# Kernel tuning notes

Hardware: AMD Instinct MI355X
Metric: run time of the kernel (lower is better)

## Reference

```python
import jax, jax.numpy as jnp
import numpy as np

H_DIM = 2048
N_HEADS = 16
HEAD_DIM = H_DIM // N_HEADS
B, S = 2, 2048


def setup_inputs() -> dict:
    key = jax.random.key(0)
    ks = jax.random.split(key, 10)
    sc = 1.0 / np.sqrt(H_DIM)
    return {
        "X": jax.random.normal(ks[0], (B, S, H_DIM), dtype=jnp.float32),
        "attention_mask": jnp.ones((B, S, S), dtype=jnp.int32),
        "Wq": jax.random.normal(ks[1], (H_DIM, H_DIM), dtype=jnp.float32) * sc,
        "bq": jnp.zeros((H_DIM,), dtype=jnp.float32),
        "Wk": jax.random.normal(ks[2], (H_DIM, H_DIM), dtype=jnp.float32) * sc,
        "bk": jnp.zeros((H_DIM,), dtype=jnp.float32),
        "Wv": jax.random.normal(ks[3], (H_DIM, H_DIM), dtype=jnp.float32) * sc,
        "bv": jnp.zeros((H_DIM,), dtype=jnp.float32),
        "Wo": jax.random.normal(ks[4], (H_DIM, H_DIM), dtype=jnp.float32) * sc,
        "bo": jnp.zeros((H_DIM,), dtype=jnp.float32),
    }


def reference(X, attention_mask, Wq, bq, Wk, bk, Wv, bv, Wo, bo):
    b, s, _ = X.shape
    # QKV projections -> [b, heads, s, head_dim]
    def proj(W, bias):
        y = jnp.einsum("bsd,de->bse", X, W) + bias
        return y.reshape(b, s, N_HEADS, HEAD_DIM).transpose(0, 2, 1, 3)
    Q, K, V = proj(Wq, bq), proj(Wk, bk), proj(Wv, bv)
    # scores [b, h, s, s]
    scores = jnp.einsum("bhqd,bhkd->bhqk", Q, K) / jnp.sqrt(jnp.float32(HEAD_DIM))
    mask = attention_mask[:, None, :, :]  # [b,1,s,s]
    scores = jnp.where(mask == 0, jnp.float32(-jnp.inf), scores)
    attn = jax.nn.softmax(scores, axis=-1)
    # dropout_rate = 0.0 -> no-op
    out = jnp.einsum("bhqk,bhkd->bhqd", attn, V)
    out = out.transpose(0, 2, 1, 3).reshape(b, s, H_DIM)
    return jnp.einsum("bsd,de->bse", out, Wo) + bo
```

## Files before the change

kernel.cpp:

```cpp
#include <hip/hip_runtime.h>
#include <hip/hip_bf16.h>

#define H_DIM 2048
#define N_HEADS 16
#define HEAD_DIM 128
#define BATCH 2
#define SEQ 2048

typedef __bf16 bf16_t;
typedef __bf16 bf16x8 __attribute__((ext_vector_type(8)));
typedef float f32x4 __attribute__((ext_vector_type(4)));

#define MFMA16(a, b, c) __builtin_amdgcn_mfma_f32_16x16x32_bf16((a), (b), (c), 0, 0, 0)

#define GLOAD16(gp, lp) __builtin_amdgcn_global_load_lds( \
    (const __attribute__((address_space(1))) void*)(gp),  \
    (__attribute__((address_space(3))) void*)(lp), 16, 0, 0)

#define WAIT_VM6()  asm volatile("s_waitcnt vmcnt(6)" ::: "memory")
#define WAIT_VM4()  asm volatile("s_waitcnt vmcnt(4)" ::: "memory")
#define WAIT_VM0()  asm volatile("s_waitcnt vmcnt(0)" ::: "memory")
#define RAW_BARRIER() asm volatile("s_barrier" ::: "memory")

__global__ __launch_bounds__(256) void detect_kernel(const unsigned int* __restrict__ X,
                                                     int* __restrict__ flags) {
    __shared__ int cnt[256];
    int t = threadIdx.x;
    int c = 0;
    for (int i = 0; i < 16; i++) {
        unsigned w  = X[t * 16 + i];
        unsigned lo = w & 0xFFFFu;
        unsigned e  = (lo >> 7) & 0xFFu;
        if (lo == 0u || (e >= 100u && e <= 141u)) c++;
    }
    cnt[t] = c;
    __syncthreads();
    for (int s = 128; s > 0; s >>= 1) {
        if (t < s) cnt[t] += cnt[t + s];
        __syncthreads();
    }
    if (t == 0) { flags[0] = (cnt[0] >= 2048) ? 1 : 0; flags[1] = 1; }
}

__global__ __launch_bounds__(256) void maskcheck_kernel(const int* __restrict__ mask,
                                                        int* __restrict__ flags) {
    size_t i = ((size_t)blockIdx.x * 256 + threadIdx.x) * 8;
    const int4* p = (const int4*)(mask + i);
    int4 a = p[0], b = p[1];
    int all = (a.x != 0) & (a.y != 0) & (a.z != 0) & (a.w != 0) &
              (b.x != 0) & (b.y != 0) & (b.z != 0) & (b.w != 0);
    if (!all) atomicAnd(&flags[1], 0);
}

__device__ inline bf16x8 load8(const void* __restrict__ p, size_t idx, int isbf16) {
    if (isbf16) {
        return *(const bf16x8*)((const bf16_t*)p + idx);
    } else {
        const float* f = (const float*)p + idx;
        float4 a = *(const float4*)f;
        float4 b = *(const float4*)(f + 4);
        bf16x8 r;
        r[0] = (bf16_t)a.x; r[1] = (bf16_t)a.y; r[2] = (bf16_t)a.z; r[3] = (bf16_t)a.w;
        r[4] = (bf16_t)b.x; r[5] = (bf16_t)b.y; r[6] = (bf16_t)b.z; r[7] = (bf16_t)b.w;
        return r;
    }
}

__device__ inline float readf(const void* __restrict__ p, int idx, int isbf16) {
    return isbf16 ? (float)((const bf16_t*)p)[idx] : ((const float*)p)[idx];
}

__global__ __launch_bounds__(256) void convert_kernel(const void* __restrict__ X,
                                                      bf16_t* __restrict__ Xb,
                                                      const int* __restrict__ flags) {
    const int isbf16 = flags[0];
    size_t i = ((size_t)blockIdx.x * 256 + threadIdx.x) * 8;
    bf16x8 v = load8(X, i, isbf16);
    *(bf16x8*)(Xb + i) = v;
}

__global__ __launch_bounds__(256) void transpose_kernel(
    const void* __restrict__ W0, const void* __restrict__ W1,
    const void* __restrict__ W2, const void* __restrict__ W3,
    bf16_t* __restrict__ Wts, const int* __restrict__ flags)
{
    const int isbf16 = flags[0];
    const int z = blockIdx.z;
    const void* W = (z == 0) ? W0 : (z == 1) ? W1 : (z == 2) ? W2 : W3;
    bf16_t* out = Wts + (size_t)z * H_DIM * H_DIM;

    __shared__ __attribute__((aligned(16))) bf16_t Ts[64][72];
    const int tid = threadIdx.x;
    const int n0 = blockIdx.x * 64;
    const int k0 = blockIdx.y * 64;

    #pragma unroll
    for (int j = 0; j < 2; j++) {
        int idx = j * 2048 + tid * 8;
        int r = idx >> 6, c = idx & 63;
        bf16x8 v = load8(W, (size_t)(k0 + r) * H_DIM + n0 + c, isbf16);
        *(bf16x8*)(&Ts[r][c]) = v;
    }
    __syncthreads();
    const int wr = tid & 63;
    const int wcg = (tid >> 6) * 8;
    #pragma unroll
    for (int j = 0; j < 2; j++) {
        int wc = wcg + j * 32;
        bf16x8 o;
        #pragma unroll
        for (int u = 0; u < 8; u++) o[u] = Ts[wc + u][wr];
        *(bf16x8*)(&out[(size_t)(n0 + wr) * H_DIM + k0 + wc]) = o;
    }
}

__global__ __launch_bounds__(256, 2) void gemm_qkv_kernel(
    const bf16_t* __restrict__ A, const bf16_t* __restrict__ Wts,
    const void* __restrict__ b0, const void* __restrict__ b1, const void* __restrict__ b2,
    bf16_t* __restrict__ qws, bf16_t* __restrict__ kws, bf16_t* __restrict__ vtws,
    const int* __restrict__ flags)
{
    const int isbf16 = flags[0];
    const int L    = blockIdx.x;
    const int xcd  = L & 7;
    const int j    = L >> 3;
    const int c    = xcd * 6 + (j % 6);
    const int mrow = j / 6;
    const int z    = c >> 4;
    const int m0   = mrow * 256;
    const int n0   = (c & 15) * 128;

    const bf16_t* Wt = Wts + (size_t)z * H_DIM * H_DIM;
    const void* bias = (z == 0) ? b0 : (z == 1) ? b1 : b2;
    bf16_t* dst = (z == 0) ? qws : (z == 1) ? kws : vtws;

    __shared__ __attribute__((aligned(16))) bf16_t As[3][4][256][8];
    __shared__ __attribute__((aligned(16))) bf16_t Bs[3][4][128][8];

    const int tid  = threadIdx.x;
    const int lane = tid & 63;
    const int wid  = tid >> 6;
    const int quad = lane >> 4;
    const int l16  = lane & 15;
    const int wm   = (wid >> 1) * 128;
    const int wn   = (wid & 1) * 64;

    f32x4 acc[8][4] = {};

    auto stage = [&](int k0, int sb) {
        #pragma unroll
        for (int jj = 0; jj < 4; jj++) {
            int slot = jj * 256 + tid;
            int k8 = slot >> 8, row = slot & 255;
            GLOAD16(A + (size_t)(m0 + row) * H_DIM + k0 + k8 * 8,
                    (bf16_t*)(&As[sb][0][0][0]) + slot * 8);
        }
        #pragma unroll
        for (int jj = 0; jj < 2; jj++) {
            int slot = jj * 256 + tid;
            int k8 = slot >> 7, row = slot & 127;
            GLOAD16(Wt + (size_t)(n0 + row) * H_DIM + k0 + k8 * 8,
                    (bf16_t*)(&Bs[sb][0][0][0]) + slot * 8);
        }
    };

    auto body = [&](int it, int bb, int sb, int mode) {
        if (mode == 2) { WAIT_VM0(); } else { WAIT_VM6(); }
        RAW_BARRIER();
        if (mode == 0) stage((it + 2) * 32, sb);
        bf16x8 bfr[4];
        #pragma unroll
        for (int i = 0; i < 4; i++)
            bfr[i] = *(const bf16x8*)(&Bs[bb][quad][wn + i * 16 + l16][0]);
        #pragma unroll
        for (int mi = 0; mi < 8; mi++) {
            bf16x8 af = *(const bf16x8*)(&As[bb][quad][wm + mi * 16 + l16][0]);
            #pragma unroll
            for (int ni = 0; ni < 4; ni++)
                acc[mi][ni] = MFMA16(af, bfr[ni], acc[mi][ni]);
        }
    };

    stage(0, 0);
    stage(32, 1);
    for (int base = 0; base < 60; base += 3) {
        body(base,     0, 2, 0);
        body(base + 1, 1, 0, 0);
        body(base + 2, 2, 1, 0);
    }
    body(60, 0, 2, 0);
    body(61, 1, 0, 0);
    body(62, 2, 1, 1);
    body(63, 0, 0, 2);

    #pragma unroll
    for (int ni = 0; ni < 4; ni++) {
        int col = n0 + wn + ni * 16 + l16;
        int h = col >> 7, d = col & (HEAD_DIM - 1);
        float bv = readf(bias, col, isbf16);
        #pragma unroll
        for (int mi = 0; mi < 8; mi++) {
            int row0 = m0 + wm + mi * 16 + quad * 4;
            int b = row0 >> 11;
            if (z < 2) {
                #pragma unroll
                for (int r = 0; r < 4; r++) {
                    int s = (row0 + r) & (SEQ - 1);
                    dst[((size_t)(b * N_HEADS + h) * SEQ + s) * HEAD_DIM + d] =
                        (bf16_t)(acc[mi][ni][r] + bv);
                }
            } else {
                int s0 = row0 & (SEQ - 1);
                bf16_t o[4];
                #pragma unroll
                for (int r = 0; r < 4; r++) o[r] = (bf16_t)(acc[mi][ni][r] + bv);
                *(unsigned long long*)(&dst[((size_t)(b * N_HEADS + h) * HEAD_DIM + d) * SEQ + s0]) =
                    *(unsigned long long*)o;
            }
        }
    }
}

__global__ __launch_bounds__(256) void gemm_out_kernel(
    const bf16_t* __restrict__ A, const bf16_t* __restrict__ Wt,
    const void* __restrict__ bias, void* __restrict__ C,
    const int* __restrict__ flags)
{
    const int isbf16 = flags[0];
    const int L    = blockIdx.x;
    const int xcd  = L & 7;
    const int j    = L >> 3;
    const int m0   = (j >> 1) * 128;
    const int n0   = (xcd * 2 + (j & 1)) * 128;

    __shared__ __attribute__((aligned(16))) bf16_t As[3][4][128][8];
    __shared__ __attribute__((aligned(16))) bf16_t Bs[3][4][128][8];

    const int tid  = threadIdx.x;
    const int lane = tid & 63;
    const int wid  = tid >> 6;
    const int quad = lane >> 4;
    const int l16  = lane & 15;
    const int wm   = (wid >> 1) * 64;
    const int wn   = (wid & 1) * 64;

    f32x4 acc[4][4] = {};

    auto stage = [&](int k0, int sb) {
        #pragma unroll
        for (int jj = 0; jj < 2; jj++) {
            int slot = jj * 256 + tid;
            int k8 = slot >> 7, row = slot & 127;
            GLOAD16(A  + (size_t)(m0 + row) * H_DIM + k0 + k8 * 8,
                    (bf16_t*)(&As[sb][0][0][0]) + slot * 8);
            GLOAD16(Wt + (size_t)(n0 + row) * H_DIM + k0 + k8 * 8,
                    (bf16_t*)(&Bs[sb][0][0][0]) + slot * 8);
        }
    };

    auto body = [&](int it, int bb, int sb, int mode) {
        if (mode == 2) { WAIT_VM0(); } else { WAIT_VM4(); }
        RAW_BARRIER();
        if (mode == 0) stage((it + 2) * 32, sb);
        bf16x8 af[4], bfr[4];
        #pragma unroll
        for (int i = 0; i < 4; i++) {
            af[i]  = *(const bf16x8*)(&As[bb][quad][wm + i * 16 + l16][0]);
            bfr[i] = *(const bf16x8*)(&Bs[bb][quad][wn + i * 16 + l16][0]);
        }
        #pragma unroll
        for (int mi = 0; mi < 4; mi++)
            #pragma unroll
            for (int ni = 0; ni < 4; ni++)
                acc[mi][ni] = MFMA16(af[mi], bfr[ni], acc[mi][ni]);
    };

    stage(0, 0);
    stage(32, 1);
    for (int base = 0; base < 60; base += 3) {
        body(base,     0, 2, 0);
        body(base + 1, 1, 0, 0);
        body(base + 2, 2, 1, 0);
    }
    body(60, 0, 2, 0);
    body(61, 1, 0, 0);
    body(62, 2, 1, 1);
    body(63, 0, 0, 2);

    #pragma unroll
    for (int ni = 0; ni < 4; ni++) {
        int col = n0 + wn + ni * 16 + l16;
        float bv = readf(bias, col, isbf16);
        #pragma unroll
        for (int mi = 0; mi < 4; mi++) {
            int row0 = m0 + wm + mi * 16 + quad * 4;
            #pragma unroll
            for (int r = 0; r < 4; r++) {
                float v = acc[mi][ni][r] + bv;
                if (isbf16) ((bf16_t*)C)[(size_t)(row0 + r) * H_DIM + col] = (bf16_t)v;
                else        ((float*)C)[(size_t)(row0 + r) * H_DIM + col]  = v;
            }
        }
    }
}

__global__ __launch_bounds__(256, 2) void attn_kernel(
    const bf16_t* __restrict__ Q, const bf16_t* __restrict__ K,
    const bf16_t* __restrict__ Vt, const int* __restrict__ mask,
    const int* __restrict__ flags, bf16_t* __restrict__ ctx)
{
    __shared__ __attribute__((aligned(16))) bf16_t Ks[2][16][64][8];
    __shared__ __attribute__((aligned(16))) bf16_t Vs[2][8][128][8];
    __shared__ __attribute__((aligned(16))) bf16_t Pl[4][16][72];

    const int tid  = threadIdx.x;
    const int lane = tid & 63;
    const int wid  = tid >> 6;
    const int quad = lane >> 4;
    const int l16  = lane & 15;

    const int bh = blockIdx.y;
    const int b  = bh >> 4, h = bh & 15;
    const int q0 = blockIdx.x * 128 + wid * 16;
    const int q1 = q0 + 64;
    const int maskAll = flags[1];

    const bf16_t* Qp = Q  + (size_t)bh * SEQ * HEAD_DIM;
    const bf16_t* Kp = K  + (size_t)bh * SEQ * HEAD_DIM;
    const bf16_t* Vp = Vt + (size_t)bh * HEAD_DIM * SEQ;
    const int*    mp = mask + (size_t)b * SEQ * SEQ;

    bf16x8 qf[2][4];
    #pragma unroll
    for (int t = 0; t < 4; t++) {
        qf[0][t] = *(const bf16x8*)(Qp + (size_t)(q0 + l16) * HEAD_DIM + t * 32 + quad * 8);
        qf[1][t] = *(const bf16x8*)(Qp + (size_t)(q1 + l16) * HEAD_DIM + t * 32 + quad * 8);
    }

    bf16x8 onesf;
    #pragma unroll
    for (int u = 0; u < 8; u++) onesf[u] = (bf16_t)1.0f;

    const float CS = 0.1275260013f;
    const float M0 = 16.0f;
    f32x4 l_acc[2] = {};
    f32x4 o_acc[2][8] = {};

    auto stage = [&](int kt, int bb) {
        const int key0 = kt * 64;
        #pragma unroll
        for (int jj = 0; jj < 4; jj++) {
            int slot = jj * 256 + tid;
            int krow = slot & 63, k8 = slot >> 6;
            GLOAD16(Kp + (size_t)(key0 + krow) * HEAD_DIM + k8 * 8,
                    (bf16_t*)(&Ks[bb][0][0][0]) + slot * 8);
        }
        #pragma unroll
        for (int jj = 0; jj < 4; jj++) {
            int slot = jj * 256 + tid;
            int d = slot & 127, kq = slot >> 7;
            GLOAD16(Vp + (size_t)d * SEQ + key0 + kq * 8,
                    (bf16_t*)(&Vs[bb][0][0][0]) + slot * 8);
        }
    };

    const int NKT = SEQ / 64;

    auto abody = [&](int kt, int bb) {
        const int key0 = kt * 64;
        __syncthreads();
        if (kt + 1 < NKT) stage(kt + 1, bb ^ 1);

        f32x4 s0[4] = {}, s1[4] = {};
        #pragma unroll
        for (int nt = 0; nt < 4; nt++) {
            #pragma unroll
            for (int t = 0; t < 4; t++) {
                bf16x8 kf = *(const bf16x8*)(&Ks[bb][t * 4 + quad][nt * 16 + l16][0]);
                s0[nt] = MFMA16(qf[0][t], kf, s0[nt]);
                s1[nt] = MFMA16(qf[1][t], kf, s1[nt]);
            }
        }

        #pragma unroll
        for (int u = 0; u < 2; u++) {
            float p2[4][4];
            #pragma unroll
            for (int nt = 0; nt < 4; nt++)
                #pragma unroll
                for (int r = 0; r < 4; r++)
                    p2[nt][r] = (u ? s1[nt][r] : s0[nt][r]) * CS - M0;

            if (!maskAll) {
                int qb = u ? q1 : q0;
                #pragma unroll
                for (int nt = 0; nt < 4; nt++) {
                    int key = key0 + nt * 16 + l16;
                    #pragma unroll
                    for (int r = 0; r < 4; r++) {
                        int q = qb + quad * 4 + r;
                        if (mp[(size_t)q * SEQ + key] == 0) p2[nt][r] = -1e30f;
                    }
                }
            }

            #pragma unroll
            for (int nt = 0; nt < 4; nt++)
                #pragma unroll
                for (int r = 0; r < 4; r++)
                    Pl[wid][quad * 4 + r][nt * 16 + l16] = (bf16_t)exp2f(p2[nt][r]);

            #pragma unroll
            for (int t = 0; t < 2; t++) {
                bf16x8 pf = *(const bf16x8*)(&Pl[wid][l16][t * 32 + quad * 8]);
                l_acc[u] = MFMA16(pf, onesf, l_acc[u]);
                #pragma unroll
                for (int dn = 0; dn < 8; dn++) {
                    bf16x8 vf = *(const bf16x8*)(&Vs[bb][t * 4 + quad][dn * 16 + l16][0]);
                    o_acc[u][dn] = MFMA16(pf, vf, o_acc[u][dn]);
                }
            }
        }
    };

    stage(0, 0);
    for (int base = 0; base < NKT; base += 2) {
        abody(base, 0);
        abody(base + 1, 1);
    }

    #pragma unroll
    for (int u = 0; u < 2; u++) {
        int qb = u ? q1 : q0;
        #pragma unroll
        for (int dn = 0; dn < 8; dn++) {
            #pragma unroll
            for (int r = 0; r < 4; r++) {
                int q = qb + quad * 4 + r;
                int d = dn * 16 + l16;
                float v = o_acc[u][dn][r] / l_acc[u][r];
                ctx[((size_t)(b * SEQ + q) * N_HEADS + h) * HEAD_DIM + d] = (bf16_t)v;
            }
        }
    }
}

extern "C" void kernel_launch(void* const* d_in, const int* in_sizes, int n_in,
                              void* d_out, int out_size, void* d_ws, size_t ws_size,
                              hipStream_t stream) {
    const void* X    = d_in[0];
    const int*  mask = (const int*)d_in[1];
    const void* Wq   = d_in[2];
    const void* bq   = d_in[3];
    const void* Wk   = d_in[4];
    const void* bk   = d_in[5];
    const void* Wv   = d_in[6];
    const void* bv   = d_in[7];
    const void* Wo   = d_in[8];
    const void* bo   = d_in[9];

    const size_t NE = (size_t)BATCH * SEQ * H_DIM;
    const size_t NW = (size_t)H_DIM * H_DIM;

    int*    flags = (int*)d_ws;
    bf16_t* Xb    = (bf16_t*)((char*)d_ws + 256);
    bf16_t* Wts   = Xb + NE;
    bf16_t* qws   = Wts + 4 * NW;
    bf16_t* kws   = qws + NE;
    bf16_t* vtws  = kws + NE;
    bf16_t* cws   = vtws + NE;

    detect_kernel<<<1, 256, 0, stream>>>((const unsigned int*)X, flags);
    maskcheck_kernel<<<(BATCH * SEQ * SEQ) / (256 * 8), 256, 0, stream>>>(mask, flags);
    convert_kernel<<<NE / (256 * 8), 256, 0, stream>>>(X, Xb, flags);
    transpose_kernel<<<dim3(32, 32, 4), 256, 0, stream>>>(Wq, Wk, Wv, Wo, Wts, flags);
    gemm_qkv_kernel<<<768, 256, 0, stream>>>(Xb, Wts, bq, bk, bv, qws, kws, vtws, flags);
    attn_kernel<<<dim3(SEQ / 128, BATCH * N_HEADS), 256, 0, stream>>>(
        qws, kws, vtws, mask, flags, cws);
    gemm_out_kernel<<<512, 256, 0, stream>>>(cws, Wts + 3 * NW, bo, d_out, flags);
}
```

Before: 575.9 us.

## Simplify GEMM loops, fuse mask check into convert, transpose attention output MFMA

Both projection GEMMs drop the triple-buffered async staging with manual vmcnt waits. They now use a single LDS buffer with two __syncthreads per k-step. The QKV GEMM tile shrinks from 256 to 128 rows, doubling its grid to 1536 blocks and lifting the two-blocks-per-CU launch bound. The mask-all-ones check is merged into the X conversion kernel to save a launch. The attention P·V and row-sum MFMAs swap operands so each lane can write four contiguous context values with one 64-bit store. The cost is losing the overlap of global loads with MFMA work in the GEMMs.

```diff
diff --git a/kernel.cpp b/kernel.cpp
--- a/kernel.cpp
+++ b/kernel.cpp
@@ -10,17 +10,13 @@
 typedef __bf16 bf16_t;
 typedef __bf16 bf16x8 __attribute__((ext_vector_type(8)));
 typedef float f32x4 __attribute__((ext_vector_type(4)));
+typedef unsigned long long u64_t;
 
 #define MFMA16(a, b, c) __builtin_amdgcn_mfma_f32_16x16x32_bf16((a), (b), (c), 0, 0, 0)
 
 #define GLOAD16(gp, lp) __builtin_amdgcn_global_load_lds( \
     (const __attribute__((address_space(1))) void*)(gp),  \
     (__attribute__((address_space(3))) void*)(lp), 16, 0, 0)
-
-#define WAIT_VM6()  asm volatile("s_waitcnt vmcnt(6)" ::: "memory")
-#define WAIT_VM4()  asm volatile("s_waitcnt vmcnt(4)" ::: "memory")
-#define WAIT_VM0()  asm volatile("s_waitcnt vmcnt(0)" ::: "memory")
-#define RAW_BARRIER() asm volatile("s_barrier" ::: "memory")
 
 __global__ __launch_bounds__(256) void detect_kernel(const unsigned int* __restrict__ X,
                                                      int* __restrict__ flags) {
@@ -40,16 +36,6 @@
         __syncthreads();
     }
     if (t == 0) { flags[0] = (cnt[0] >= 2048) ? 1 : 0; flags[1] = 1; }
-}
-
-__global__ __launch_bounds__(256) void maskcheck_kernel(const int* __restrict__ mask,
-                                                        int* __restrict__ flags) {
-    size_t i = ((size_t)blockIdx.x * 256 + threadIdx.x) * 8;
-    const int4* p = (const int4*)(mask + i);
-    int4 a = p[0], b = p[1];
-    int all = (a.x != 0) & (a.y != 0) & (a.z != 0) & (a.w != 0) &
-              (b.x != 0) & (b.y != 0) & (b.z != 0) & (b.w != 0);
-    if (!all) atomicAnd(&flags[1], 0);
 }
 
 __device__ inline bf16x8 load8(const void* __restrict__ p, size_t idx, int isbf16) {
@@ -70,13 +56,20 @@
     return isbf16 ? (float)((const bf16_t*)p)[idx] : ((const float*)p)[idx];
 }
 
-__global__ __launch_bounds__(256) void convert_kernel(const void* __restrict__ X,
-                                                      bf16_t* __restrict__ Xb,
-                                                      const int* __restrict__ flags) {
+__global__ __launch_bounds__(256) void convert_mask_kernel(
+    const void* __restrict__ X, bf16_t* __restrict__ Xb,
+    const int* __restrict__ mask, int* __restrict__ flags)
+{
     const int isbf16 = flags[0];
     size_t i = ((size_t)blockIdx.x * 256 + threadIdx.x) * 8;
     bf16x8 v = load8(X, i, isbf16);
     *(bf16x8*)(Xb + i) = v;
+
+    const int4* p = (const int4*)(mask + i);
+    int4 a = p[0], b = p[1];
+    int all = (a.x != 0) & (a.y != 0) & (a.z != 0) & (a.w != 0) &
+              (b.x != 0) & (b.y != 0) & (b.z != 0) & (b.w != 0);
+    if (!all) atomicAnd(&flags[1], 0);
 }
 
 __global__ __launch_bounds__(256) void transpose_kernel(
@@ -114,7 +107,7 @@
     }
 }
 
-__global__ __launch_bounds__(256, 2) void gemm_qkv_kernel(
+__global__ __launch_bounds__(256) void gemm_qkv_kernel(
     const bf16_t* __restrict__ A, const bf16_t* __restrict__ Wts,
     const void* __restrict__ b0, const void* __restrict__ b1, const void* __restrict__ b2,
     bf16_t* __restrict__ qws, bf16_t* __restrict__ kws, bf16_t* __restrict__ vtws,
@@ -127,71 +120,48 @@
     const int c    = xcd * 6 + (j % 6);
     const int mrow = j / 6;
     const int z    = c >> 4;
-    const int m0   = mrow * 256;
+    const int m0   = mrow * 128;
     const int n0   = (c & 15) * 128;
 
     const bf16_t* Wt = Wts + (size_t)z * H_DIM * H_DIM;
     const void* bias = (z == 0) ? b0 : (z == 1) ? b1 : b2;
     bf16_t* dst = (z == 0) ? qws : (z == 1) ? kws : vtws;
 
-    __shared__ __attribute__((aligned(16))) bf16_t As[3][4][256][8];
-    __shared__ __attribute__((aligned(16))) bf16_t Bs[3][4][128][8];
+    __shared__ __attribute__((aligned(16))) bf16_t As[4][128][8];
+    __shared__ __attribute__((aligned(16))) bf16_t Bs[4][128][8];
 
     const int tid  = threadIdx.x;
     const int lane = tid & 63;
     const int wid  = tid >> 6;
     const int quad = lane >> 4;
     const int l16  = lane & 15;
-    const int wm   = (wid >> 1) * 128;
+    const int wm   = (wid >> 1) * 64;
     const int wn   = (wid & 1) * 64;
 
-    f32x4 acc[8][4] = {};
-
-    auto stage = [&](int k0, int sb) {
-        #pragma unroll
-        for (int jj = 0; jj < 4; jj++) {
-            int slot = jj * 256 + tid;
-            int k8 = slot >> 8, row = slot & 255;
-            GLOAD16(A + (size_t)(m0 + row) * H_DIM + k0 + k8 * 8,
-                    (bf16_t*)(&As[sb][0][0][0]) + slot * 8);
-        }
+    f32x4 acc[4][4] = {};
+
+    for (int k0 = 0; k0 < H_DIM; k0 += 32) {
         #pragma unroll
         for (int jj = 0; jj < 2; jj++) {
             int slot = jj * 256 + tid;
             int k8 = slot >> 7, row = slot & 127;
-            GLOAD16(Wt + (size_t)(n0 + row) * H_DIM + k0 + k8 * 8,
-                    (bf16_t*)(&Bs[sb][0][0][0]) + slot * 8);
-        }
-    };
-
-    auto body = [&](int it, int bb, int sb, int mode) {
-        if (mode == 2) { WAIT_VM0(); } else { WAIT_VM6(); }
-        RAW_BARRIER();
-        if (mode == 0) stage((it + 2) * 32, sb);
-        bf16x8 bfr[4];
-        #pragma unroll
-        for (int i = 0; i < 4; i++)
-            bfr[i] = *(const bf16x8*)(&Bs[bb][quad][wn + i * 16 + l16][0]);
-        #pragma unroll
-        for (int mi = 0; mi < 8; mi++) {
-            bf16x8 af = *(const bf16x8*)(&As[bb][quad][wm + mi * 16 + l16][0]);
+            GLOAD16(A  + (size_t)(m0 + row) * H_DIM + k0 + k8 * 8, (bf16_t*)As + slot * 8);
+            GLOAD16(Wt + (size_t)(n0 + row) * H_DIM + k0 + k8 * 8, (bf16_t*)Bs + slot * 8);
+        }
+        __syncthreads();
+        bf16x8 af[4], bfr[4];
+        #pragma unroll
+        for (int i = 0; i < 4; i++) {
+            af[i]  = *(const bf16x8*)(&As[quad][wm + i * 16 + l16][0]);
+            bfr[i] = *(const bf16x8*)(&Bs[quad][wn + i * 16 + l16][0]);
+        }
+        #pragma unroll
+        for (int mi = 0; mi < 4; mi++)
             #pragma unroll
             for (int ni = 0; ni < 4; ni++)
-                acc[mi][ni] = MFMA16(af, bfr[ni], acc[mi][ni]);
-        }
-    };
-
-    stage(0, 0);
-    stage(32, 1);
-    for (int base = 0; base < 60; base += 3) {
-        body(base,     0, 2, 0);
-        body(base + 1, 1, 0, 0);
-        body(base + 2, 2, 1, 0);
-    }
-    body(60, 0, 2, 0);
-    body(61, 1, 0, 0);
-    body(62, 2, 1, 1);
-    body(63, 0, 0, 2);
+                acc[mi][ni] = MFMA16(af[mi], bfr[ni], acc[mi][ni]);
+        __syncthreads();
+    }
 
     #pragma unroll
     for (int ni = 0; ni < 4; ni++) {
@@ -199,7 +169,7 @@
         int h = col >> 7, d = col & (HEAD_DIM - 1);
         float bv = readf(bias, col, isbf16);
         #pragma unroll
-        for (int mi = 0; mi < 8; mi++) {
+        for (int mi = 0; mi < 4; mi++) {
             int row0 = m0 + wm + mi * 16 + quad * 4;
             int b = row0 >> 11;
             if (z < 2) {
@@ -214,8 +184,8 @@
                 bf16_t o[4];
                 #pragma unroll
                 for (int r = 0; r < 4; r++) o[r] = (bf16_t)(acc[mi][ni][r] + bv);
-                *(unsigned long long*)(&dst[((size_t)(b * N_HEADS + h) * HEAD_DIM + d) * SEQ + s0]) =
-                    *(unsigned long long*)o;
+                *(u64_t*)(&dst[((size_t)(b * N_HEADS + h) * HEAD_DIM + d) * SEQ + s0]) =
+                    *(u64_t*)o;
             }
         }
     }
@@ -233,8 +203,8 @@
     const int m0   = (j >> 1) * 128;
     const int n0   = (xcd * 2 + (j & 1)) * 128;
 
-    __shared__ __attribute__((aligned(16))) bf16_t As[3][4][128][8];
-    __shared__ __attribute__((aligned(16))) bf16_t Bs[3][4][128][8];
+    __shared__ __attribute__((aligned(16))) bf16_t As[4][128][8];
+    __shared__ __attribute__((aligned(16))) bf16_t Bs[4][128][8];
 
     const int tid  = threadIdx.x;
     const int lane = tid & 63;
@@ -246,46 +216,28 @@
 
     f32x4 acc[4][4] = {};
 
-    auto stage = [&](int k0, int sb) {
+    for (int k0 = 0; k0 < H_DIM; k0 += 32) {
         #pragma unroll
         for (int jj = 0; jj < 2; jj++) {
             int slot = jj * 256 + tid;
             int k8 = slot >> 7, row = slot & 127;
-            GLOAD16(A  + (size_t)(m0 + row) * H_DIM + k0 + k8 * 8,
-                    (bf16_t*)(&As[sb][0][0][0]) + slot * 8);
-            GLOAD16(Wt + (size_t)(n0 + row) * H_DIM + k0 + k8 * 8,
-                    (bf16_t*)(&Bs[sb][0][0][0]) + slot * 8);
-        }
-    };
-
-    auto body = [&](int it, int bb, int sb, int mode) {
-        if (mode == 2) { WAIT_VM0(); } else { WAIT_VM4(); }
-        RAW_BARRIER();
-        if (mode == 0) stage((it + 2) * 32, sb);
+            GLOAD16(A  + (size_t)(m0 + row) * H_DIM + k0 + k8 * 8, (bf16_t*)As + slot * 8);
+            GLOAD16(Wt + (size_t)(n0 + row) * H_DIM + k0 + k8 * 8, (bf16_t*)Bs + slot * 8);
+        }
+        __syncthreads();
         bf16x8 af[4], bfr[4];
         #pragma unroll
         for (int i = 0; i < 4; i++) {
-            af[i]  = *(const bf16x8*)(&As[bb][quad][wm + i * 16 + l16][0]);
-            bfr[i] = *(const bf16x8*)(&Bs[bb][quad][wn + i * 16 + l16][0]);
+            af[i]  = *(const bf16x8*)(&As[quad][wm + i * 16 + l16][0]);
+            bfr[i] = *(const bf16x8*)(&Bs[quad][wn + i * 16 + l16][0]);
         }
         #pragma unroll
         for (int mi = 0; mi < 4; mi++)
             #pragma unroll
             for (int ni = 0; ni < 4; ni++)
                 acc[mi][ni] = MFMA16(af[mi], bfr[ni], acc[mi][ni]);
-    };
-
-    stage(0, 0);
-    stage(32, 1);
-    for (int base = 0; base < 60; base += 3) {
-        body(base,     0, 2, 0);
-        body(base + 1, 1, 0, 0);
-        body(base + 2, 2, 1, 0);
-    }
-    body(60, 0, 2, 0);
-    body(61, 1, 0, 0);
-    body(62, 2, 1, 1);
-    body(63, 0, 0, 2);
+        __syncthreads();
+    }
 
     #pragma unroll
     for (int ni = 0; ni < 4; ni++) {
@@ -413,11 +365,11 @@
             #pragma unroll
             for (int t = 0; t < 2; t++) {
                 bf16x8 pf = *(const bf16x8*)(&Pl[wid][l16][t * 32 + quad * 8]);
-                l_acc[u] = MFMA16(pf, onesf, l_acc[u]);
+                l_acc[u] = MFMA16(onesf, pf, l_acc[u]);
                 #pragma unroll
                 for (int dn = 0; dn < 8; dn++) {
                     bf16x8 vf = *(const bf16x8*)(&Vs[bb][t * 4 + quad][dn * 16 + l16][0]);
-                    o_acc[u][dn] = MFMA16(pf, vf, o_acc[u][dn]);
+                    o_acc[u][dn] = MFMA16(vf, pf, o_acc[u][dn]);
                 }
             }
         }
@@ -432,15 +384,14 @@
     #pragma unroll
     for (int u = 0; u < 2; u++) {
         int qb = u ? q1 : q0;
+        float inv = 1.0f / l_acc[u][0];
+        bf16_t* cp = ctx + ((size_t)(b * SEQ + qb + l16)) * H_DIM + h * HEAD_DIM;
         #pragma unroll
         for (int dn = 0; dn < 8; dn++) {
-            #pragma unroll
-            for (int r = 0; r < 4; r++) {
-                int q = qb + quad * 4 + r;
-                int d = dn * 16 + l16;
-                float v = o_acc[u][dn][r] / l_acc[u][r];
-                ctx[((size_t)(b * SEQ + q) * N_HEADS + h) * HEAD_DIM + d] = (bf16_t)v;
-            }
+            bf16_t o4[4];
+            #pragma unroll
+            for (int r = 0; r < 4; r++) o4[r] = (bf16_t)(o_acc[u][dn][r] * inv);
+            *(u64_t*)(cp + dn * 16 + quad * 4) = *(u64_t*)o4;
         }
     }
 }
@@ -471,10 +422,9 @@
     bf16_t* cws   = vtws + NE;
 
     detect_kernel<<<1, 256, 0, stream>>>((const unsigned int*)X, flags);
-    maskcheck_kernel<<<(BATCH * SEQ * SEQ) / (256 * 8), 256, 0, stream>>>(mask, flags);
-    convert_kernel<<<NE / (256 * 8), 256, 0, stream>>>(X, Xb, flags);
+    convert_mask_kernel<<<NE / (256 * 8), 256, 0, stream>>>(X, Xb, mask, flags);
     transpose_kernel<<<dim3(32, 32, 4), 256, 0, stream>>>(Wq, Wk, Wv, Wo, Wts, flags);
-    gemm_qkv_kernel<<<768, 256, 0, stream>>>(Xb, Wts, bq, bk, bv, qws, kws, vtws, flags);
+    gemm_qkv_kernel<<<1536, 256, 0, stream>>>(Xb, Wts, bq, bk, bv, qws, kws, vtws, flags);
     attn_kernel<<<dim3(SEQ / 128, BATCH * N_HEADS), 256, 0, stream>>>(
         qws, kws, vtws, mask, flags, cws);
     gemm_out_kernel<<<512, 256, 0, stream>>>(cws, Wts + 3 * NW, bo, d_out, flags);
```

New measurement: 588.2 us. +2.1%, slower.
